# Kernel optimization log

Hardware: AMD Instinct MI355X
Metric: run time of the kernel (lower is better)

Reference implementation:

```python
import jax, jax.numpy as jnp
import numpy as np

N, D, H, L = 16384, 512, 64, 7  # nodes, feature dim, hidden, num labels


def setup_inputs() -> dict:
    key = jax.random.key(0)
    ks = jax.random.split(key, 6)
    matrix = jax.random.randint(ks[0], (N, N), 0, 2).astype(jnp.float32)  # dense binary adjacency
    x_features = jax.random.normal(ks[1], (N, D), dtype=jnp.float32)
    x_labels = jax.random.randint(ks[2], (N, L), 0, 2).astype(jnp.int32)  # multi-hot labels
    W2 = jax.random.normal(ks[3], (D, H), dtype=jnp.float32) / np.float32(np.sqrt(D))
    b2 = jnp.zeros((H,), jnp.float32)
    Wp = jax.random.normal(ks[4], (D, L), dtype=jnp.float32) / np.float32(np.sqrt(D))
    bp = jnp.zeros((L,), jnp.float32)
    return {"matrix": matrix, "x_features": x_features, "W2": W2, "b2": b2,
            "Wp": Wp, "bp": bp, "x_labels": x_labels, "index": 123, "flag": 2}


def reference(matrix, x_features, W2, b2, Wp, bp, x_labels, index, flag):
    # Implements the flag != 1 path (trans2 -> labelwise aggregation -> maxpool -> predict).
    assert flag == 2
    z = x_features @ W2 + b2                      # [N, 64]  (trans2 over all nodes)
    row = matrix[index]                           # [N] binary neighbor mask of node `index`
    deg = matrix.sum(axis=1)                      # [N] degrees of all nodes
    # para_j = 1/sqrt(deg_j * deg_index) for neighbors, 0 otherwise (row is the mask)
    para = row / jnp.sqrt(deg * row.sum())        # [N]
    lab = x_labels.astype(z.dtype)                # [N, 7]
    # label-wise degree-normalized neighbor aggregation: tmp_a[i] = sum_j para_j * lab[j,i] * z[j]
    tmp_a = jnp.einsum('n,nl,nd->ld', para, lab, z)   # [7, 64]
    h = jax.nn.relu(jnp.concatenate([z[index], tmp_a.reshape(-1)])[None, :])  # [1, 512]
    # stack + MaxPool1d(2) over the pair == elementwise max
    h_combi = jnp.maximum(x_features[index][None, :], h)  # [1, 512]
    out = h_combi @ Wp + bp                        # [1, 7]
    return out
```

## Files before the change

kernel.cpp:

```cpp
#include <hip/hip_runtime.h>

#define NN 16384
#define DD 512
#define HH 64
#define LL 7
#define NAGG 256
#define JPB  (NN / NAGG)

typedef float f32x4 __attribute__((ext_vector_type(4)));

#define WS_QV 0
#define WS_S  16384
#define WS_CP 16400
#define WS_GP 20480

__global__ void k_deg(const float* __restrict__ matrix,
                      const int* __restrict__ pidx,
                      float* __restrict__ qv) {
    __shared__ float sdata[4];
    int j = blockIdx.x;
    int t = threadIdx.x;
    int lane = t & 63;
    int wid = t >> 6;
    int idx = *pidx;
    float m = matrix[(size_t)idx * NN + j];
    if (m == 0.f) {
        if (t == 0) qv[j] = 0.f;
        return;
    }
    const f32x4* r4 = (const f32x4*)(matrix + (size_t)j * NN);
    float v0 = 0.f, v1 = 0.f, v2 = 0.f, v3 = 0.f;
    #pragma unroll
    for (int it = 0; it < 4; ++it) {
        f32x4 a  = __builtin_nontemporal_load(&r4[t + (it * 4 + 0) * 256]);
        f32x4 b  = __builtin_nontemporal_load(&r4[t + (it * 4 + 1) * 256]);
        f32x4 cc = __builtin_nontemporal_load(&r4[t + (it * 4 + 2) * 256]);
        f32x4 d  = __builtin_nontemporal_load(&r4[t + (it * 4 + 3) * 256]);
        v0 += a.x + a.y + a.z + a.w;
        v1 += b.x + b.y + b.z + b.w;
        v2 += cc.x + cc.y + cc.z + cc.w;
        v3 += d.x + d.y + d.z + d.w;
    }
    float v = (v0 + v1) + (v2 + v3);
    #pragma unroll
    for (int off = 32; off > 0; off >>= 1)
        v += __shfl_down(v, off);
    if (lane == 0) sdata[wid] = v;
    __syncthreads();
    if (t == 0) {
        float deg = (sdata[0] + sdata[1]) + (sdata[2] + sdata[3]);
        qv[j] = rsqrtf(deg);
    }
}

__global__ void k_agg(const float* __restrict__ matrix,
                      const float* __restrict__ xf,
                      const int* __restrict__ lab,
                      const int* __restrict__ pidx,
                      const float* __restrict__ bp,
                      const float* __restrict__ qv,
                      float* __restrict__ gpart,
                      float* __restrict__ cpart,
                      float* __restrict__ Sout,
                      float* __restrict__ out) {
    __shared__ float sS[4];
    int t = threadIdx.x;
    int b = blockIdx.x;
    int d0 = t * 2;
    float2 acc[LL];
    #pragma unroll
    for (int l = 0; l < LL; ++l) acc[l] = make_float2(0.f, 0.f);
    float cacc[LL] = {0.f, 0.f, 0.f, 0.f, 0.f, 0.f, 0.f};

    #pragma unroll 1
    for (int trip = 0; trip < JPB / 4; ++trip) {
        int jj[4];
        float qq[4];
        #pragma unroll
        for (int k = 0; k < 4; ++k) {
            jj[k] = b + (trip * 4 + k) * NAGG;
            qq[k] = qv[jj[k]];
        }
        #pragma unroll
        for (int k = 0; k < 4; ++k) {
            if (qq[k] != 0.f) {
                float2 xv = *(const float2*)(xf + (size_t)jj[k] * DD + d0);
                float wl[LL];
                #pragma unroll
                for (int l = 0; l < LL; ++l)
                    wl[l] = qq[k] * (float)lab[jj[k] * LL + l];
                #pragma unroll
                for (int l = 0; l < LL; ++l) {
                    acc[l].x = fmaf(wl[l], xv.x, acc[l].x);
                    acc[l].y = fmaf(wl[l], xv.y, acc[l].y);
                }
                #pragma unroll
                for (int l = 0; l < LL; ++l) cacc[l] += wl[l];
            }
        }
    }
    #pragma unroll
    for (int l = 0; l < LL; ++l)
        *(float2*)(gpart + ((size_t)b * LL + l) * DD + d0) = acc[l];
    if (t == 0) {
        #pragma unroll
        for (int l = 0; l < LL; ++l) cpart[b * 8 + l] = cacc[l];
    }
    if (b == 0) {
        int idx = *pidx;
        const f32x4* r4 = (const f32x4*)(matrix + (size_t)idx * NN);
        float v = 0.f;
        #pragma unroll
        for (int it = 0; it < 16; ++it) {
            f32x4 a = r4[t + it * 256];
            v += a.x + a.y + a.z + a.w;
        }
        #pragma unroll
        for (int off = 32; off > 0; off >>= 1)
            v += __shfl_down(v, off);
        if ((t & 63) == 0) sS[t >> 6] = v;
        __syncthreads();
        if (t == 0) {
            Sout[0] = (sS[0] + sS[1]) + (sS[2] + sS[3]);
            #pragma unroll
            for (int l = 0; l < LL; ++l) out[l] = bp[l];
        }
    }
}

__global__ void k_final(const float* __restrict__ xf,
                        const float* __restrict__ W2,
                        const float* __restrict__ b2,
                        const float* __restrict__ Wp,
                        const int* __restrict__ pidx,
                        const float* __restrict__ gpart,
                        const float* __restrict__ cpart,
                        const float* __restrict__ Sf,
                        float* __restrict__ out) {
    __shared__ float gl[DD];
    __shared__ float csd[4];
    __shared__ float csum_s;
    __shared__ float out_acc[LL];
    int t = threadIdx.x;
    int b = blockIdx.x;
    int lane = t & 63;
    int wid = t >> 6;
    int idx = *pidx;

    if (b >= 1) {
        int l = b - 1;
        float2 s = make_float2(0.f, 0.f);
        const float* gbase = gpart + (size_t)l * DD + t * 2;
        #pragma unroll 8
        for (int pb = 0; pb < NAGG; ++pb) {
            float2 v = *(const float2*)(gbase + (size_t)pb * (LL * DD));
            s.x += v.x; s.y += v.y;
        }
        gl[t * 2] = s.x;
        gl[t * 2 + 1] = s.y;
        float cv = cpart[t * 8 + l];
        #pragma unroll
        for (int off = 32; off > 0; off >>= 1)
            cv += __shfl_down(cv, off);
        if (lane == 0) csd[wid] = cv;
    }
    if (t < LL) out_acc[t] = 0.f;
    __syncthreads();
    if (b >= 1 && t == 0)
        csum_s = (csd[0] + csd[1]) + (csd[2] + csd[3]);
    __syncthreads();

    int p = b * 64 + (t >> 2);
    int sub = t & 3;
    int h = (b == 0) ? p : (p - HH) & 63;
    int dbase = sub * 128;
    const float* src = (b == 0) ? (xf + (size_t)idx * DD) : gl;
    float s0 = 0.f, s1 = 0.f, s2 = 0.f, s3 = 0.f;
    #pragma unroll 8
    for (int d = 0; d < 128; d += 4) {
        s0 = fmaf(src[dbase + d],     W2[(dbase + d)     * HH + h], s0);
        s1 = fmaf(src[dbase + d + 1], W2[(dbase + d + 1) * HH + h], s1);
        s2 = fmaf(src[dbase + d + 2], W2[(dbase + d + 2) * HH + h], s2);
        s3 = fmaf(src[dbase + d + 3], W2[(dbase + d + 3) * HH + h], s3);
    }
    float v = (s0 + s1) + (s2 + s3);
    v += __shfl_down(v, 2);
    v += __shfl_down(v, 1);

    if (sub == 0) {
        float val;
        if (b == 0) {
            val = v + b2[p];
        } else {
            float sc = rsqrtf(Sf[0]);
            val = (v + csum_s * b2[h]) * sc;
        }
        float relu_v = val > 0.f ? val : 0.f;
        float hc = fmaxf(xf[(size_t)idx * DD + p], relu_v);
        #pragma unroll
        for (int o = 0; o < LL; ++o)
            atomicAdd(&out_acc[o], hc * Wp[p * LL + o]);
    }
    __syncthreads();
    if (t < LL) atomicAdd(&out[t], out_acc[t]);
}

extern "C" void kernel_launch(void* const* d_in, const int* in_sizes, int n_in,
                              void* d_out, int out_size, void* d_ws, size_t ws_size,
                              hipStream_t stream) {
    const float* matrix = (const float*)d_in[0];
    const float* xf     = (const float*)d_in[1];
    const float* W2     = (const float*)d_in[2];
    const float* b2     = (const float*)d_in[3];
    const float* Wp     = (const float*)d_in[4];
    const float* bp     = (const float*)d_in[5];
    const int*   lab    = (const int*)d_in[6];
    const int*   pidx   = (const int*)d_in[7];
    float* outp = (float*)d_out;
    float* wsf  = (float*)d_ws;

    k_deg<<<NN, 256, 0, stream>>>(matrix, pidx, wsf + WS_QV);
    k_agg<<<NAGG, 256, 0, stream>>>(matrix, xf, lab, pidx, bp, wsf + WS_QV,
                                    wsf + WS_GP, wsf + WS_CP, wsf + WS_S, outp);
    k_final<<<8, 256, 0, stream>>>(xf, W2, b2, Wp, pidx,
                                   wsf + WS_GP, wsf + WS_CP, wsf + WS_S, outp);
}
```

Measured before the change: 135.4 us.

## Batch rows per block in degree kernel and split final reduction across waves

The degree kernel now launches 4096 blocks, each handling 4 strided rows gated by the index row, instead of one block per row. This cuts launch and block-scheduling overhead and lets one block keep several row loads in flight. The aggregation loop batches 8 neighbor rows per trip instead of 4 for more memory-level parallelism. The final kernel splits the 256-partial reduction across 4 waves, writes per-wave sums to shared memory and then combines them. Fewer blocks in the degree pass could lower occupancy or cause load imbalance, since about half the rows are skipped.

```diff
diff --git a/kernel.cpp b/kernel.cpp
--- a/kernel.cpp
+++ b/kernel.cpp
@@ -6,6 +6,8 @@
 #define LL 7
 #define NAGG 256
 #define JPB  (NN / NAGG)
+#define DEGB 4096
+#define RPB  (NN / DEGB)
 
 typedef float f32x4 __attribute__((ext_vector_type(4)));
 
@@ -17,39 +19,54 @@
 __global__ void k_deg(const float* __restrict__ matrix,
                       const int* __restrict__ pidx,
                       float* __restrict__ qv) {
-    __shared__ float sdata[4];
-    int j = blockIdx.x;
+    __shared__ float sdata[RPB][4];
     int t = threadIdx.x;
     int lane = t & 63;
     int wid = t >> 6;
     int idx = *pidx;
-    float m = matrix[(size_t)idx * NN + j];
-    if (m == 0.f) {
-        if (t == 0) qv[j] = 0.f;
-        return;
-    }
-    const f32x4* r4 = (const f32x4*)(matrix + (size_t)j * NN);
-    float v0 = 0.f, v1 = 0.f, v2 = 0.f, v3 = 0.f;
-    #pragma unroll
-    for (int it = 0; it < 4; ++it) {
-        f32x4 a  = __builtin_nontemporal_load(&r4[t + (it * 4 + 0) * 256]);
-        f32x4 b  = __builtin_nontemporal_load(&r4[t + (it * 4 + 1) * 256]);
-        f32x4 cc = __builtin_nontemporal_load(&r4[t + (it * 4 + 2) * 256]);
-        f32x4 d  = __builtin_nontemporal_load(&r4[t + (it * 4 + 3) * 256]);
-        v0 += a.x + a.y + a.z + a.w;
-        v1 += b.x + b.y + b.z + b.w;
-        v2 += cc.x + cc.y + cc.z + cc.w;
-        v3 += d.x + d.y + d.z + d.w;
-    }
-    float v = (v0 + v1) + (v2 + v3);
-    #pragma unroll
-    for (int off = 32; off > 0; off >>= 1)
-        v += __shfl_down(v, off);
-    if (lane == 0) sdata[wid] = v;
-    __syncthreads();
-    if (t == 0) {
-        float deg = (sdata[0] + sdata[1]) + (sdata[2] + sdata[3]);
-        qv[j] = rsqrtf(deg);
+    int j0 = blockIdx.x;
+
+    float gate[RPB];
+    #pragma unroll
+    for (int k = 0; k < RPB; ++k)
+        gate[k] = matrix[(size_t)idx * NN + j0 + k * DEGB];
+
+    float vsum[RPB];
+    #pragma unroll
+    for (int k = 0; k < RPB; ++k) vsum[k] = 0.f;
+
+    #pragma unroll
+    for (int k = 0; k < RPB; ++k) {
+        if (gate[k] != 0.f) {
+            const f32x4* r4 = (const f32x4*)(matrix + (size_t)(j0 + k * DEGB) * NN);
+            float v0 = 0.f, v1 = 0.f, v2 = 0.f, v3 = 0.f;
+            #pragma unroll
+            for (int it = 0; it < 4; ++it) {
+                f32x4 a  = __builtin_nontemporal_load(&r4[t + (it * 4 + 0) * 256]);
+                f32x4 b  = __builtin_nontemporal_load(&r4[t + (it * 4 + 1) * 256]);
+                f32x4 cc = __builtin_nontemporal_load(&r4[t + (it * 4 + 2) * 256]);
+                f32x4 d  = __builtin_nontemporal_load(&r4[t + (it * 4 + 3) * 256]);
+                v0 += a.x + a.y + a.z + a.w;
+                v1 += b.x + b.y + b.z + b.w;
+                v2 += cc.x + cc.y + cc.z + cc.w;
+                v3 += d.x + d.y + d.z + d.w;
+            }
+            vsum[k] = (v0 + v1) + (v2 + v3);
+        }
+    }
+
+    #pragma unroll
+    for (int k = 0; k < RPB; ++k) {
+        float v = vsum[k];
+        #pragma unroll
+        for (int off = 32; off > 0; off >>= 1)
+            v += __shfl_down(v, off);
+        if (lane == 0) sdata[k][wid] = v;
+    }
+    __syncthreads();
+    if (t < RPB) {
+        float deg = (sdata[t][0] + sdata[t][1]) + (sdata[t][2] + sdata[t][3]);
+        qv[j0 + t * DEGB] = deg > 0.f ? rsqrtf(deg) : 0.f;
     }
 }
 
@@ -73,16 +90,16 @@
     float cacc[LL] = {0.f, 0.f, 0.f, 0.f, 0.f, 0.f, 0.f};
 
     #pragma unroll 1
-    for (int trip = 0; trip < JPB / 4; ++trip) {
-        int jj[4];
-        float qq[4];
-        #pragma unroll
-        for (int k = 0; k < 4; ++k) {
-            jj[k] = b + (trip * 4 + k) * NAGG;
+    for (int trip = 0; trip < JPB / 8; ++trip) {
+        int jj[8];
+        float qq[8];
+        #pragma unroll
+        for (int k = 0; k < 8; ++k) {
+            jj[k] = b + (trip * 8 + k) * NAGG;
             qq[k] = qv[jj[k]];
         }
         #pragma unroll
-        for (int k = 0; k < 4; ++k) {
+        for (int k = 0; k < 8; ++k) {
             if (qq[k] != 0.f) {
                 float2 xv = *(const float2*)(xf + (size_t)jj[k] * DD + d0);
                 float wl[LL];
@@ -137,6 +154,7 @@
                         const float* __restrict__ cpart,
                         const float* __restrict__ Sf,
                         float* __restrict__ out) {
+    __shared__ float glp[4][DD];
     __shared__ float gl[DD];
     __shared__ float csd[4];
     __shared__ float csum_s;
@@ -149,15 +167,24 @@
 
     if (b >= 1) {
         int l = b - 1;
-        float2 s = make_float2(0.f, 0.f);
-        const float* gbase = gpart + (size_t)l * DD + t * 2;
-        #pragma unroll 8
-        for (int pb = 0; pb < NAGG; ++pb) {
-            float2 v = *(const float2*)(gbase + (size_t)pb * (LL * DD));
-            s.x += v.x; s.y += v.y;
-        }
-        gl[t * 2] = s.x;
-        gl[t * 2 + 1] = s.y;
+        float2 s[4];
+        #pragma unroll
+        for (int q = 0; q < 4; ++q) s[q] = make_float2(0.f, 0.f);
+        #pragma unroll 4
+        for (int pbi = 0; pbi < NAGG / 4; ++pbi) {
+            int pb = wid * (NAGG / 4) + pbi;
+            const float* gb = gpart + ((size_t)pb * LL + l) * DD;
+            #pragma unroll
+            for (int q = 0; q < 4; ++q) {
+                float2 v = *(const float2*)(gb + (lane + q * 64) * 2);
+                s[q].x += v.x; s[q].y += v.y;
+            }
+        }
+        #pragma unroll
+        for (int q = 0; q < 4; ++q) {
+            glp[wid][(lane + q * 64) * 2]     = s[q].x;
+            glp[wid][(lane + q * 64) * 2 + 1] = s[q].y;
+        }
         float cv = cpart[t * 8 + l];
         #pragma unroll
         for (int off = 32; off > 0; off >>= 1)
@@ -166,8 +193,14 @@
     }
     if (t < LL) out_acc[t] = 0.f;
     __syncthreads();
-    if (b >= 1 && t == 0)
-        csum_s = (csd[0] + csd[1]) + (csd[2] + csd[3]);
+
+    if (b >= 1) {
+        gl[t * 2]     = ((glp[0][t * 2]     + glp[1][t * 2])
+                       + (glp[2][t * 2]     + glp[3][t * 2]));
+        gl[t * 2 + 1] = ((glp[0][t * 2 + 1] + glp[1][t * 2 + 1])
+                       + (glp[2][t * 2 + 1] + glp[3][t * 2 + 1]));
+        if (t == 0) csum_s = (csd[0] + csd[1]) + (csd[2] + csd[3]);
+    }
     __syncthreads();
 
     int p = b * 64 + (t >> 2);
@@ -219,7 +252,7 @@
     float* outp = (float*)d_out;
     float* wsf  = (float*)d_ws;
 
-    k_deg<<<NN, 256, 0, stream>>>(matrix, pidx, wsf + WS_QV);
+    k_deg<<<DEGB, 256, 0, stream>>>(matrix, pidx, wsf + WS_QV);
     k_agg<<<NAGG, 256, 0, stream>>>(matrix, xf, lab, pidx, bp, wsf + WS_QV,
                                     wsf + WS_GP, wsf + WS_CP, wsf + WS_S, outp);
     k_final<<<8, 256, 0, stream>>>(xf, W2, b2, Wp, pidx,
```

After: 134.5 us (median of 2 runs). No clear change (-0.7%).
